# Kernel tuning notes

Measured on AMD Instinct MI355X. Metric: run time of the kernel, lower is better.

The kernel has to match this reference:

```python
import jax, jax.numpy as jnp
from jax import lax
import numpy as np

D_MODEL = 1024
EXPAND = 2
D_INNER = D_MODEL * EXPAND
D_STATE = 16
D_CONV = 4
DECAY = 0.95
LN_EPS = 1e-5


def setup_inputs() -> dict:
    key = jax.random.key(0)
    ks = jax.random.split(key, 9)
    b, s = 4, 2048
    scale = 1.0 / np.sqrt(D_MODEL)
    inner_scale = 1.0 / np.sqrt(D_INNER)
    return {
        "x": jax.random.normal(ks[0], (b, s, D_MODEL), dtype=jnp.float32),
        "W_in": jax.random.normal(ks[1], (2 * D_INNER, D_MODEL), dtype=jnp.float32) * scale,
        "conv_w": jax.random.normal(ks[2], (D_INNER, 1, D_CONV), dtype=jnp.float32) * 0.5,
        "conv_b": jax.random.normal(ks[3], (D_INNER,), dtype=jnp.float32) * 0.1,
        "W_x": jax.random.normal(ks[4], (2 * D_STATE, D_INNER), dtype=jnp.float32) * inner_scale,
        "B_log": jax.random.normal(ks[5], (D_INNER, D_STATE), dtype=jnp.float32) * 0.05,  # xavier-ish small
        "W_out": jax.random.normal(ks[6], (D_MODEL, D_INNER), dtype=jnp.float32) * inner_scale,
        "ln_g": jnp.ones((D_MODEL,), dtype=jnp.float32),
        "ln_b": jnp.zeros((D_MODEL,), dtype=jnp.float32),
    }


def _ssm_block(x, W_in, conv_w, conv_b, W_x, B_log, W_out, ln_g, ln_b):
    b, s, _ = x.shape
    d_inner = W_in.shape[0] // 2
    d_conv = conv_w.shape[-1]

    # input projection and gate split
    xz = jnp.einsum('bsd,ed->bse', x, W_in)            # [b, s, 2*d_inner]
    x_inner, z = jnp.split(xz, 2, axis=-1)             # each [b, s, d_inner]

    # causal depthwise conv (left pad d_conv-1, output length s)
    xc = jnp.transpose(x_inner, (0, 2, 1))             # [b, d_inner, s]
    conv = lax.conv_general_dilated(
        xc, conv_w, window_strides=(1,), padding=[(d_conv - 1, 0)],
        feature_group_count=d_inner)
    conv = conv + conv_b[None, :, None]
    x_conv = jax.nn.silu(jnp.transpose(conv, (0, 2, 1)))  # [b, s, d_inner]

    # selective parameters; s_B is produced but unused in the original math
    sp = jnp.einsum('bsd,nd->bsn', x_conv, W_x)        # [b, s, 2*d_state]
    _s_B, s_C = jnp.split(sp, 2, axis=-1)              # each [b, s, d_state]

    B = jnp.exp(B_log)                                  # [d_inner, d_state]

    # state_t = 0.95*state_{t-1} + B * x_t  factorizes as  state = B[d,n]*h[b,t,d]
    # with h_t = 0.95*h_{t-1} + x_conv_t ; scan over time with [b, d_inner] carry.
    def step(h, xt):
        h = DECAY * h + xt
        return h, h

    h0 = jnp.zeros((b, d_inner), dtype=x.dtype)
    _, h = lax.scan(step, h0, jnp.swapaxes(x_conv, 0, 1))  # [s, b, d_inner]
    h = jnp.swapaxes(h, 0, 1)                              # [b, s, d_inner]

    # output_t[b,d] = sum_n state[b,d,n]*s_C[b,t,n] = h[b,t,d] * (s_C @ B^T)[b,t,d]
    y = h * jnp.einsum('bsn,dn->bsd', s_C, B)
    y = y * jax.nn.silu(z)
    y = jnp.einsum('bsd,od->bso', y, W_out)            # [b, s, d_model]

    resid = x + y
    mu = jnp.mean(resid, axis=-1, keepdims=True)
    var = jnp.var(resid, axis=-1, keepdims=True)
    return (resid - mu) * lax.rsqrt(var + LN_EPS) * ln_g + ln_b


def reference(x, W_in, conv_w, conv_b, W_x, B_log, W_out, ln_g, ln_b):
    return _ssm_block(x, W_in, conv_w, conv_b, W_x, B_log, W_out, ln_g, ln_b)
```

## Files before the change

kernel.cpp:

```cpp
#include <hip/hip_runtime.h>
#include <hip/hip_bf16.h>
#include <stdint.h>

#define DM   1024
#define DI   2048
#define NST  16
#define BSZ  4
#define SLEN 2048
#define MROWS (BSZ*SLEN)
#define CHUNK 32
#define NCH  (SLEN/CHUNK)
#define DECAYF 0.95f
#define MB (size_t)1048576

typedef _Float16 f16;
typedef __attribute__((ext_vector_type(2))) _Float16 f16x2;
typedef __attribute__((ext_vector_type(4))) _Float16 f16x4;
typedef __attribute__((ext_vector_type(8))) _Float16 f16x8;
typedef __attribute__((ext_vector_type(4))) float f32x4;

__device__ __forceinline__ float silu_f(float v) { return v / (1.f + __expf(-v)); }

__device__ __forceinline__ void gload16(const f16* lds, const f16* g) {
  __builtin_amdgcn_global_load_lds((const __attribute__((address_space(1))) void*)g,
                                   (__attribute__((address_space(3))) void*)lds, 16, 0, 0);
}

#define NX4  (MROWS * DM / 4)
#define NWI4 (2 * DI * DM / 4)
#define NWO4 (DM * DI / 4)
#define NWX4 (NST * DI / 4)
#define NE4  (NST * DI / 4)
__global__ __launch_bounds__(256) void cvt_all(
    const float* __restrict__ x, const float* __restrict__ wi, const float* __restrict__ wo,
    const float* __restrict__ Wx, const float* __restrict__ B_log,
    f16* __restrict__ A1, f16* __restrict__ B1, f16* __restrict__ W2,
    f16* __restrict__ WxC, f16* __restrict__ expBT)
{
  int i = blockIdx.x * 256 + threadIdx.x;
  if (i < NX4 + NWI4 + NWO4 + NWX4) {
    const float* src; f16* dst; int j;
    if (i < NX4)                     { src = x;  dst = A1; j = i; }
    else if (i < NX4 + NWI4)         { src = wi; dst = B1; j = i - NX4; }
    else if (i < NX4 + NWI4 + NWO4)  { src = wo; dst = W2; j = i - NX4 - NWI4; }
    else                             { src = Wx + (size_t)NST * DI; dst = WxC; j = i - NX4 - NWI4 - NWO4; }
    float4 v = ((const float4*)src)[j];
    f16x4 o = {(f16)v.x, (f16)v.y, (f16)v.z, (f16)v.w};
    ((f16x4*)dst)[j] = o;
  } else {
    int j = i - NX4 - NWI4 - NWO4 - NWX4;
    int base = j * 4;
    int n = base >> 11, d = base & (DI - 1);
    f16x4 o = {(f16)__expf(B_log[(d + 0) * NST + n]), (f16)__expf(B_log[(d + 1) * NST + n]),
               (f16)__expf(B_log[(d + 2) * NST + n]), (f16)__expf(B_log[(d + 3) * NST + n])};
    ((f16x4*)expBT)[j] = o;
  }
}

template<int MODE>
__global__ __launch_bounds__(256) void gemm_bt(
    const f16* __restrict__ A, const f16* __restrict__ Bt,
    int K, f16* __restrict__ O0, f16* __restrict__ O1)
{
  __shared__ __align__(16) f16 sA[128 * 64];
  __shared__ __align__(16) f16 sB[128 * 64];
  const int tid  = threadIdx.x;
  const int lane = tid & 63;
  const int w    = tid >> 6;
  const int wr   = w >> 1, wc = w & 1;

  const int nwg  = gridDim.x * gridDim.y;
  int wgid = blockIdx.y * gridDim.x + blockIdx.x;
  wgid = (wgid & 7) * (nwg >> 3) + (wgid >> 3);
  const int bx = wgid % gridDim.x;
  const int by = wgid / gridDim.x;

  const int mBase = by * 128;
  const int nBase = bx * 128;
  const int lr = lane & 15;
  const int lu = lane >> 4;

  f32x4 acc[4][4];
  #pragma unroll
  for (int m = 0; m < 4; ++m)
    #pragma unroll
    for (int n = 0; n < 4; ++n)
      acc[m][n] = (f32x4){0.f, 0.f, 0.f, 0.f};

  int offA[4][2], offB[4][2];
  #pragma unroll
  for (int m = 0; m < 4; ++m) {
    int ra = wr * 64 + m * 16 + lr;
    int rb = wc * 64 + m * 16 + lr;
    #pragma unroll
    for (int kk = 0; kk < 2; ++kk) {
      offA[m][kk] = ra * 64 + ((kk * 4 + lu) ^ (ra & 7)) * 8;
      offB[m][kk] = rb * 64 + ((kk * 4 + lu) ^ (rb & 7)) * 8;
    }
  }

  for (int k0 = 0; k0 < K; k0 += 64) {
    #pragma unroll
    for (int j = 0; j < 4; ++j) {
      int c = j * 256 + tid;
      int row = c >> 3, p = c & 7;
      int su = p ^ (row & 7);
      gload16(&sA[c * 8], A  + (size_t)(mBase + row) * K + k0 + su * 8);
      gload16(&sB[c * 8], Bt + (size_t)(nBase + row) * K + k0 + su * 8);
    }
    __syncthreads();
    #pragma unroll
    for (int kk = 0; kk < 2; ++kk) {
      f16x8 af[4], bf[4];
      #pragma unroll
      for (int m = 0; m < 4; ++m) af[m] = *(const f16x8*)&sA[offA[m][kk]];
      #pragma unroll
      for (int n = 0; n < 4; ++n) bf[n] = *(const f16x8*)&sB[offB[n][kk]];
      #pragma unroll
      for (int m = 0; m < 4; ++m)
        #pragma unroll
        for (int n = 0; n < 4; ++n)
          acc[m][n] = __builtin_amdgcn_mfma_f32_16x16x32_f16(af[m], bf[n], acc[m][n], 0, 0, 0);
    }
    __syncthreads();
  }

  const int rq = (lane >> 4) * 4;
  f16* sOut = sA;
  const bool isZ = (MODE == 1) && (nBase >= DI);
  f16* dst = (MODE == 0) ? O0 : (isZ ? O1 : O0);
  const int ncols = (MODE == 0) ? DM : DI;
  const int cb = isZ ? (nBase - DI) : nBase;
  #pragma unroll
  for (int m = 0; m < 4; ++m) {
    #pragma unroll
    for (int n = 0; n < 4; ++n)
      #pragma unroll
      for (int r = 0; r < 4; ++r)
        sOut[(wr * 16 + rq + r) * 128 + wc * 64 + n * 16 + lr] = (f16)acc[m][n][r];
    __syncthreads();
    #pragma unroll
    for (int q = 0; q < 2; ++q) {
      int cidx = q * 256 + tid;
      int orow = cidx >> 4;
      int ocol = (cidx & 15) * 8;
      int grow = mBase + (orow >> 4) * 64 + m * 16 + (orow & 15);
      f16x8 v = *(const f16x8*)&sOut[orow * 128 + ocol];
      *(f16x8*)&dst[(size_t)grow * ncols + cb + ocol] = v;
    }
    __syncthreads();
  }
}

__global__ __launch_bounds__(256) void conv_scan(
    const f16* __restrict__ Xi, const float* __restrict__ convW, const float* __restrict__ convB,
    f16* __restrict__ Xc, f16* __restrict__ Hl, float* __restrict__ L)
{
  const int tid = threadIdx.x;
  const int d0 = (blockIdx.x * 256 + tid) * 4;
  const int ch = blockIdx.y;
  const int b  = blockIdx.z;
  const int t0 = ch * CHUNK;

  float w0[4], w1[4], w2[4], w3[4], cb[4];
  #pragma unroll
  for (int i = 0; i < 4; ++i) {
    float4 wv = ((const float4*)convW)[d0 + i];
    w0[i] = wv.x; w1[i] = wv.y; w2[i] = wv.z; w3[i] = wv.w;
    cb[i] = convB[d0 + i];
  }

  float xm3[4], xm2[4], xm1[4];
  auto loadrow = [&](int t, float* dst) {
    if (t < 0) {
      #pragma unroll
      for (int i = 0; i < 4; ++i) dst[i] = 0.f;
      return;
    }
    f16x4 v = *(const f16x4*)&Xi[((size_t)(b * SLEN + t)) * DI + d0];
    #pragma unroll
    for (int i = 0; i < 4; ++i) dst[i] = (float)v[i];
  };
  loadrow(t0 - 3, xm3); loadrow(t0 - 2, xm2); loadrow(t0 - 1, xm1);

  float h[4] = {0.f, 0.f, 0.f, 0.f};
  for (int t = 0; t < CHUNK; ++t) {
    const size_t ro = ((size_t)(b * SLEN + t0 + t)) * DI + d0;
    f16x4 xv = *(const f16x4*)&Xi[ro];
    f16x4 xco, hho;
    #pragma unroll
    for (int i = 0; i < 4; ++i) {
      float xt = (float)xv[i];
      float c = cb[i] + w0[i]*xm3[i] + w1[i]*xm2[i] + w2[i]*xm1[i] + w3[i]*xt;
      float xc = silu_f(c);
      h[i] = DECAYF * h[i] + xc;
      xco[i] = (f16)xc;
      hho[i] = (f16)h[i];
      xm3[i] = xm2[i]; xm2[i] = xm1[i]; xm1[i] = xt;
    }
    *(f16x4*)&Xc[ro] = xco;
    *(f16x4*)&Hl[ro] = hho;
  }
  const size_t lo = ((size_t)(b * NCH + ch)) * DI + d0;
  float4 l0 = {h[0], h[1], h[2], h[3]};
  *(float4*)&L[lo] = l0;
}

__global__ void carry_scan(const float* __restrict__ L, f16* __restrict__ Carry) {
  int i = blockIdx.x * blockDim.x + threadIdx.x;
  int b = i >> 11, d = i & (DI - 1);
  float dp = 1.f;
  #pragma unroll
  for (int k = 0; k < CHUNK; ++k) dp *= DECAYF;
  float c = 0.f;
  for (int ch0 = 0; ch0 < NCH; ch0 += 8) {
    float lv[8];
    #pragma unroll
    for (int k = 0; k < 8; ++k)
      lv[k] = L[((size_t)(b * NCH + ch0 + k)) * DI + d];
    #pragma unroll
    for (int k = 0; k < 8; ++k) {
      c = dp * c + lv[k];
      Carry[((size_t)(b * NCH + ch0 + k)) * DI + d] = (f16)c;
    }
  }
}

__global__ __launch_bounds__(256) void sc_gemm(const f16* __restrict__ Xc, const f16* __restrict__ WxC,
                                               float* __restrict__ sC) {
  const int m = blockIdx.x * 4 + (threadIdx.x >> 6);
  const int lane = threadIdx.x & 63;
  float acc[16];
  #pragma unroll
  for (int n = 0; n < 16; ++n) acc[n] = 0.f;
  #pragma unroll
  for (int it = 0; it < DI / 512; ++it) {
    int d = it * 512 + lane * 8;
    f16x8 xv = *(const f16x8*)&Xc[(size_t)m * DI + d];
    #pragma unroll
    for (int n = 0; n < 16; ++n) {
      f16x8 wv = *(const f16x8*)&WxC[(size_t)n * DI + d];
      float s = 0.f;
      #pragma unroll
      for (int i = 0; i < 8; ++i) s += (float)xv[i] * (float)wv[i];
      acc[n] += s;
    }
  }
  #pragma unroll
  for (int n = 0; n < 16; ++n) {
    #pragma unroll
    for (int off = 32; off > 0; off >>= 1) acc[n] += __shfl_xor(acc[n], off);
  }
  if (lane == 0) {
    #pragma unroll
    for (int n = 0; n < 16; ++n) sC[m * 16 + n] = acc[n];
  }
}

__global__ __launch_bounds__(256) void ew_y(
    const f16* __restrict__ Hl, const f16* __restrict__ Zs,
    const float* __restrict__ sC, const f16* __restrict__ expBT,
    const f16* __restrict__ Carry, f16* __restrict__ Y)
{
  const int r = threadIdx.x >> 6, lane = threadIdx.x & 63;
  const int m = blockIdx.y * 4 + r;
  const int d0 = blockIdx.x * 512 + lane * 8;
  const int b = m >> 11, t = m & (SLEN - 1);
  const int ch = t / CHUNK, tl = t & (CHUNK - 1);

  float coef = 0.f;
  if (ch > 0) {
    coef = 1.f;
    for (int j = 0; j <= tl; ++j) coef *= DECAYF;
  }

  const float4 sc0 = *(const float4*)&sC[m * 16 + 0];
  const float4 sc1 = *(const float4*)&sC[m * 16 + 4];
  const float4 sc2 = *(const float4*)&sC[m * 16 + 8];
  const float4 sc3 = *(const float4*)&sC[m * 16 + 12];
  const float scv[16] = {sc0.x, sc0.y, sc0.z, sc0.w, sc1.x, sc1.y, sc1.z, sc1.w,
                         sc2.x, sc2.y, sc2.z, sc2.w, sc3.x, sc3.y, sc3.z, sc3.w};

  const size_t ro = (size_t)m * DI + d0;
  f16x8 hvv = *(const f16x8*)&Hl[ro];
  f16x8 zvv = *(const f16x8*)&Zs[ro];
  float hv[8], zv[8], ca[8];
  #pragma unroll
  for (int i = 0; i < 8; ++i) {
    hv[i] = (float)hvv[i];
    zv[i] = silu_f((float)zvv[i]);
    ca[i] = 0.f;
  }
  if (ch > 0) {
    const size_t co = ((size_t)(b * NCH + ch - 1)) * DI + d0;
    f16x8 cv = *(const f16x8*)&Carry[co];
    #pragma unroll
    for (int i = 0; i < 8; ++i) ca[i] = (float)cv[i];
  }

  float cp[8] = {0.f, 0.f, 0.f, 0.f, 0.f, 0.f, 0.f, 0.f};
  #pragma unroll
  for (int n = 0; n < 16; ++n) {
    f16x8 ev = *(const f16x8*)&expBT[(size_t)n * DI + d0];
    #pragma unroll
    for (int i = 0; i < 8; ++i) cp[i] += scv[n] * (float)ev[i];
  }

  f16x8 o;
  #pragma unroll
  for (int i = 0; i < 8; ++i) {
    float y = (hv[i] + coef * ca[i]) * cp[i] * zv[i];
    o[i] = (f16)y;
  }
  *(f16x8*)&Y[ro] = o;
}

__global__ __launch_bounds__(256) void ln_res(const f16* __restrict__ G, const float* __restrict__ x,
                                              const float* __restrict__ lng, const float* __restrict__ lnb,
                                              float* __restrict__ out) {
  const int m = blockIdx.x;
  const int tid = threadIdx.x;
  f16x4 gv4 = ((const f16x4*)(G + (size_t)m * DM))[tid];
  float4 xv = ((const float4*)(x + (size_t)m * DM))[tid];
  float4 rv = {(float)gv4.x + xv.x, (float)gv4.y + xv.y, (float)gv4.z + xv.z, (float)gv4.w + xv.w};
  float s = rv.x + rv.y + rv.z + rv.w;
  float s2 = rv.x * rv.x + rv.y * rv.y + rv.z * rv.z + rv.w * rv.w;
  #pragma unroll
  for (int off = 32; off > 0; off >>= 1) {
    s += __shfl_xor(s, off);
    s2 += __shfl_xor(s2, off);
  }
  __shared__ float ps[8];
  const int w = tid >> 6;
  if ((tid & 63) == 0) { ps[w] = s; ps[w + 4] = s2; }
  __syncthreads();
  float S = ps[0] + ps[1] + ps[2] + ps[3];
  float S2 = ps[4] + ps[5] + ps[6] + ps[7];
  float mu = S * (1.f / DM);
  float var = S2 * (1.f / DM) - mu * mu;
  float rs = rsqrtf(var + 1e-5f);
  float4 gg = ((const float4*)lng)[tid];
  float4 bb = ((const float4*)lnb)[tid];
  float4 ov = {(rv.x - mu) * rs * gg.x + bb.x, (rv.y - mu) * rs * gg.y + bb.y,
               (rv.z - mu) * rs * gg.z + bb.z, (rv.w - mu) * rs * gg.w + bb.w};
  ((float4*)(out + (size_t)m * DM))[tid] = ov;
}

extern "C" void kernel_launch(void* const* d_in, const int* in_sizes, int n_in,
                              void* d_out, int out_size, void* d_ws, size_t ws_size,
                              hipStream_t stream) {
  const float* x      = (const float*)d_in[0];
  const float* W_in   = (const float*)d_in[1];
  const float* conv_w = (const float*)d_in[2];
  const float* conv_b = (const float*)d_in[3];
  const float* W_x    = (const float*)d_in[4];
  const float* B_log  = (const float*)d_in[5];
  const float* W_out  = (const float*)d_in[6];
  const float* ln_g   = (const float*)d_in[7];
  const float* ln_b   = (const float*)d_in[8];
  float* out = (float*)d_out;

  char* ws = (char*)d_ws;
  f16*   Xi  = (f16*)(ws + 0);
  f16*   Yp  = (f16*)(ws + 0);
  f16*   Zs  = (f16*)(ws + 32 * MB);
  f16*   Xc  = (f16*)(ws + 64 * MB);
  f16*   Hl  = (f16*)(ws + 96 * MB);
  f16*   A1  = (f16*)(ws + 128 * MB);
  f16*   B1  = (f16*)(ws + 144 * MB);
  f16*   W2  = (f16*)(ws + 152 * MB);
  f16*   G   = (f16*)(ws + 156 * MB);
  float* L     = (float*)(ws + 172 * MB);
  f16*   Carry = (f16*)(ws + 174 * MB);
  float* sC    = (float*)(ws + 175 * MB);
  f16*   expBT = (f16*)(ws + 176 * MB);
  f16*   WxC   = (f16*)(ws + 177 * MB);

  cvt_all<<<(NX4 + NWI4 + NWO4 + NWX4 + NE4) / 256, 256, 0, stream>>>(
      x, W_in, W_out, W_x, B_log, A1, B1, W2, WxC, expBT);

  gemm_bt<1><<<dim3(2 * DI / 128, MROWS / 128), 256, 0, stream>>>(A1, B1, DM, Xi, Zs);

  conv_scan<<<dim3(DI / 1024, NCH, BSZ), 256, 0, stream>>>(Xi, conv_w, conv_b, Xc, Hl, L);
  carry_scan<<<(BSZ * DI) / 256, 256, 0, stream>>>(L, Carry);
  sc_gemm<<<MROWS / 4, 256, 0, stream>>>(Xc, WxC, sC);
  ew_y<<<dim3(DI / 512, MROWS / 4), 256, 0, stream>>>(Hl, Zs, sC, expBT, Carry, Yp);

  gemm_bt<0><<<dim3(DM / 128, MROWS / 128), 256, 0, stream>>>(Yp, W2, DI, G, nullptr);

  ln_res<<<MROWS, 256, 0, stream>>>(G, x, ln_g, ln_b, out);
}
```

Measured before the change: 254.7 us.

## Replace input-projection GEMM with 256x256-tile 8-phase pipelined kernel

Adds a dedicated input-projection GEMM that uses 256x256 output tiles with 512 threads and double-buffered LDS. Global-to-LDS loads for the next K-slices are interleaved in half-tile chunks across eight MFMA phases, with explicit vmcnt waits, barriers and setprio. The goal is to hide load latency and raise arithmetic intensity compared with the generic 128x128 kernel. In exchange it uses 128KB of LDS per block and many accumulator registers, which may limit occupancy, and the hand-written wait counts are fragile.

```diff
diff --git a/kernel.cpp b/kernel.cpp
--- a/kernel.cpp
+++ b/kernel.cpp
@@ -57,6 +57,139 @@
   }
 }
 
+#define G1K 1024
+#define G1NIT 8
+
+__device__ __forceinline__ void stage_half(const f16* __restrict__ mat, int matBase,
+                                           int kt, int h, f16* ldsDst, int tid) {
+  #pragma unroll
+  for (int q = 0; q < 2; ++q) {
+    int c = q * 512 + tid;
+    int row = h * 128 + (c >> 3);
+    int p = c & 7;
+    int su = p ^ (row & 7);
+    gload16(ldsDst + h * 8192 + c * 8,
+            mat + (size_t)(matBase + row) * G1K + kt * 64 + su * 8);
+  }
+}
+
+#define WAITV(n) asm volatile("s_waitcnt vmcnt(" #n ")" ::: "memory")
+
+__global__ __launch_bounds__(512, 2) void gemm1_8ph(
+    const f16* __restrict__ A, const f16* __restrict__ Bt,
+    f16* __restrict__ Xi, f16* __restrict__ Zs)
+{
+  __shared__ __align__(16) f16 lds[65536];
+  const int tid  = threadIdx.x;
+  const int lane = tid & 63;
+  const int w    = tid >> 6;
+  const int wr   = w >> 2, wc = w & 3;
+  const int lr   = lane & 15;
+  const int lq   = lane >> 4;
+
+  const int nwg = gridDim.x * gridDim.y;
+  int wgid = blockIdx.y * gridDim.x + blockIdx.x;
+  wgid = (wgid & 7) * (nwg >> 3) + (wgid >> 3);
+  const int bx = wgid % gridDim.x;
+  const int by = wgid / gridDim.x;
+  const int mBase = by * 256;
+  const int nBase = bx * 256;
+
+  f32x4 acc[8][4];
+  #pragma unroll
+  for (int mf = 0; mf < 8; ++mf)
+    #pragma unroll
+    for (int nf = 0; nf < 4; ++nf)
+      acc[mf][nf] = (f32x4){0.f, 0.f, 0.f, 0.f};
+
+  auto rdA = [&](int S, int mf, int kk) -> f16x8 {
+    int ra = wr * 128 + mf * 16 + lr;
+    return *(const f16x8*)&lds[S * 32768 + ra * 64 + (((kk << 2) + lq) ^ (ra & 7)) * 8];
+  };
+  auto rdB = [&](int S, int nf, int kk) -> f16x8 {
+    int rb = wc * 64 + nf * 16 + lr;
+    return *(const f16x8*)&lds[S * 32768 + 16384 + rb * 64 + (((kk << 2) + lq) ^ (rb & 7)) * 8];
+  };
+
+  f16x8 bfr[4][2], afr[2][2];
+
+#define PHASE(S, p, ISSUE, TAIL) do {                                           \
+    if ((p) == 0) {                                                             \
+      _Pragma("unroll")                                                         \
+      for (int nf = 0; nf < 4; ++nf) {                                          \
+        bfr[nf][0] = rdB((S), nf, 0); bfr[nf][1] = rdB((S), nf, 1);             \
+      }                                                                         \
+    }                                                                           \
+    afr[0][0] = rdA((S), 2 * (p), 0);     afr[0][1] = rdA((S), 2 * (p), 1);     \
+    afr[1][0] = rdA((S), 2 * (p) + 1, 0); afr[1][1] = rdA((S), 2 * (p) + 1, 1); \
+    ISSUE;                                                                      \
+    __builtin_amdgcn_s_barrier();                                               \
+    asm volatile("s_waitcnt lgkmcnt(0)" ::: "memory");                          \
+    __builtin_amdgcn_sched_barrier(0);                                          \
+    __builtin_amdgcn_s_setprio(1);                                              \
+    _Pragma("unroll")                                                           \
+    for (int mm = 0; mm < 2; ++mm)                                              \
+      _Pragma("unroll")                                                         \
+      for (int nf = 0; nf < 4; ++nf) {                                          \
+        acc[2*(p)+mm][nf] = __builtin_amdgcn_mfma_f32_16x16x32_f16(             \
+            afr[mm][0], bfr[nf][0], acc[2*(p)+mm][nf], 0, 0, 0);                \
+        acc[2*(p)+mm][nf] = __builtin_amdgcn_mfma_f32_16x16x32_f16(             \
+            afr[mm][1], bfr[nf][1], acc[2*(p)+mm][nf], 0, 0, 0);                \
+      }                                                                         \
+    __builtin_amdgcn_s_setprio(0);                                              \
+    __builtin_amdgcn_sched_barrier(0);                                          \
+    TAIL;                                                                       \
+    __builtin_amdgcn_s_barrier();                                               \
+  } while (0)
+
+  stage_half(Bt, nBase, 0, 0, &lds[16384], tid);
+  stage_half(Bt, nBase, 0, 1, &lds[16384], tid);
+  stage_half(A,  mBase, 0, 0, &lds[0],     tid);
+  stage_half(A,  mBase, 0, 1, &lds[0],     tid);
+  stage_half(Bt, nBase, 1, 0, &lds[32768 + 16384], tid);
+  stage_half(Bt, nBase, 1, 1, &lds[32768 + 16384], tid);
+  WAITV(4);
+  __builtin_amdgcn_s_barrier();
+
+  for (int j = 0; j < G1NIT; ++j) {
+    const int P = 2 * j, Q = 2 * j + 1;
+    const bool more = (j < G1NIT - 1);
+    PHASE(0, 0, stage_half(A, mBase, Q, 0, &lds[32768], tid), (void)0);
+    PHASE(0, 1, stage_half(A, mBase, Q, 1, &lds[32768], tid), (void)0);
+    PHASE(0, 2, if (more) stage_half(Bt, nBase, P + 2, 0, &lds[16384], tid), (void)0);
+    PHASE(0, 3, if (more) stage_half(Bt, nBase, P + 2, 1, &lds[16384], tid),
+                if (more) { WAITV(4); } else { WAITV(0); });
+    PHASE(1, 0, if (more) stage_half(A, mBase, P + 2, 0, &lds[0], tid), (void)0);
+    PHASE(1, 1, if (more) stage_half(A, mBase, P + 2, 1, &lds[0], tid), (void)0);
+    PHASE(1, 2, if (more) stage_half(Bt, nBase, P + 3, 0, &lds[32768 + 16384], tid), (void)0);
+    PHASE(1, 3, if (more) stage_half(Bt, nBase, P + 3, 1, &lds[32768 + 16384], tid),
+                if (more) { WAITV(4); });
+  }
+#undef PHASE
+
+  __syncthreads();
+  const int rq = lq * 4;
+  #pragma unroll
+  for (int mf = 0; mf < 8; ++mf)
+    #pragma unroll
+    for (int nf = 0; nf < 4; ++nf)
+      #pragma unroll
+      for (int r = 0; r < 4; ++r)
+        lds[(wr * 128 + mf * 16 + rq + r) * 256 + wc * 64 + nf * 16 + lr] = (f16)acc[mf][nf][r];
+  __syncthreads();
+  #pragma unroll
+  for (int it = 0; it < 16; ++it) {
+    int cidx = it * 512 + tid;
+    int row = cidx >> 5;
+    int col8 = (cidx & 31) * 8;
+    int grow = mBase + row;
+    int gcol = nBase + col8;
+    f16x8 v = *(const f16x8*)&lds[row * 256 + col8];
+    if (gcol < DI) *(f16x8*)&Xi[(size_t)grow * DI + gcol] = v;
+    else           *(f16x8*)&Zs[(size_t)grow * DI + (gcol - DI)] = v;
+  }
+}
+
 template<int MODE>
 __global__ __launch_bounds__(256) void gemm_bt(
     const f16* __restrict__ A, const f16* __restrict__ Bt,
@@ -379,7 +512,7 @@
   cvt_all<<<(NX4 + NWI4 + NWO4 + NWX4 + NE4) / 256, 256, 0, stream>>>(
       x, W_in, W_out, W_x, B_log, A1, B1, W2, WxC, expBT);
 
-  gemm_bt<1><<<dim3(2 * DI / 128, MROWS / 128), 256, 0, stream>>>(A1, B1, DM, Xi, Zs);
+  gemm1_8ph<<<dim3(2 * DI / 256, MROWS / 256), 512, 0, stream>>>(A1, B1, Xi, Zs);
 
   conv_scan<<<dim3(DI / 1024, NCH, BSZ), 256, 0, stream>>>(Xi, conv_w, conv_b, Xc, Hl, L);
   carry_scan<<<(BSZ * DI) / 256, 256, 0, stream>>>(L, Carry);
```

Measured after the change: 248.9 us. -2.3%, faster.
